# Performance work log

Measured on AMD Instinct MI355X. Metric: run time of the kernel, lower is better.

The kernel has to match this reference:

```python
import jax, jax.numpy as jnp
import numpy as np

TEMPERATURE = 0.1
EPS = 1e-12  # F.normalize eps


def setup_inputs() -> dict:
    key = jax.random.key(0)
    k1, k2 = jax.random.split(key)
    B, D = 4096, 128
    return {
        "x_i": jax.random.normal(k1, (B, D), dtype=jnp.float32),
        "x_j": jax.random.normal(k2, (B, D), dtype=jnp.float32),
    }


def _l2_normalize(x):
    n = jnp.sqrt(jnp.sum(x * x, axis=1, keepdims=True))
    return x / jnp.maximum(n, EPS)


def reference(x_i, x_j):
    B = x_i.shape[0]
    z = jnp.concatenate([_l2_normalize(x_i), _l2_normalize(x_j)], axis=0)  # [2B, D]
    # cosine similarity of unit-norm rows == dot product -> single GEMM
    sim = z @ z.T  # [2B, 2B]
    idx = jnp.arange(B)
    sim_ij = sim[idx, idx + B]   # diag(sim, +B)
    sim_ji = sim[idx + B, idx]   # diag(sim, -B)
    positives = jnp.concatenate([sim_ij, sim_ji], axis=0)  # [2B]
    neg_mask = 1.0 - jnp.eye(2 * B, dtype=sim.dtype)
    denominator = jnp.sum(neg_mask * jnp.exp(sim / TEMPERATURE), axis=1)  # [2B]
    # -log(exp(pos/t) / denom) = -(pos/t - log denom)
    loss_partial = jnp.log(denominator) - positives / TEMPERATURE
    return jnp.sum(loss_partial) / (2 * B)
```

## Files before the change

kernel.cpp:

```cpp
#include <hip/hip_runtime.h>
#include <stdint.h>

#define D_DIM 128
#define NROW 8192
#define L2EPS 1e-12f
#define SCALE_PRE 0.9495707f
#define LN2 0.6931471805599453f

typedef __attribute__((ext_vector_type(4))) int   i32x4;
typedef __attribute__((ext_vector_type(8))) int   i32x8;
typedef __attribute__((ext_vector_type(4))) float f32x4;

#define AS1 __attribute__((address_space(1)))
#define AS3 __attribute__((address_space(3)))

static __device__ inline void gload_lds16(const void* g, void* l) {
    __builtin_amdgcn_global_load_lds((const AS1 uint32_t*)g, (AS3 uint32_t*)l, 16, 0, 0);
}

static __device__ inline i32x8 cat8(i32x4 lo, i32x4 hi) {
    i32x8 r;
    r[0] = lo[0]; r[1] = lo[1]; r[2] = lo[2]; r[3] = lo[3];
    r[4] = hi[0]; r[5] = hi[1]; r[6] = hi[2]; r[7] = hi[3];
    return r;
}

static __device__ __forceinline__ float fexp2(float x) {
#if __has_builtin(__builtin_amdgcn_exp2f)
    return __builtin_amdgcn_exp2f(x);
#else
    float r;
    asm("v_exp_f32 %0, %1" : "=v"(r) : "v"(x));
    return r;
#endif
}

static __device__ __forceinline__ float dpp_row_sum16(float v) {
    union { float f; int i; } u, s;
    u.f = v;
    s.i = __builtin_amdgcn_update_dpp(0, u.i, 0x118, 0xF, 0xF, true); u.f += s.f;
    s.i = __builtin_amdgcn_update_dpp(0, u.i, 0x114, 0xF, 0xF, true); u.f += s.f;
    s.i = __builtin_amdgcn_update_dpp(0, u.i, 0x112, 0xF, 0xF, true); u.f += s.f;
    s.i = __builtin_amdgcn_update_dpp(0, u.i, 0x111, 0xF, 0xF, true); u.f += s.f;
    return u.f;
}

__global__ __launch_bounds__(256) void k_normalize(
        const float* __restrict__ xi, const float* __restrict__ xj,
        uint8_t* __restrict__ z8, float* __restrict__ rowacc,
        float* __restrict__ colacc, float* __restrict__ pos_acc,
        float* __restrict__ logsum, unsigned* __restrict__ done_ct) {
    const int wave = threadIdx.x >> 6;
    const int lane = threadIdx.x & 63;
    const int row = blockIdx.x * 4 + wave;
    const float* src = (row < 4096) ? (xi + (size_t)row * D_DIM)
                                    : (xj + (size_t)(row - 4096) * D_DIM);
    float2 v = *(const float2*)(src + lane * 2);
    float ss = v.x * v.x + v.y * v.y;
#pragma unroll
    for (int m = 32; m >= 1; m >>= 1) ss += __shfl_xor(ss, m, 64);
    const float scale = SCALE_PRE / fmaxf(sqrtf(ss), L2EPS);
    const int pk = __builtin_amdgcn_cvt_pk_fp8_f32(v.x * scale, v.y * scale, 0, false);
    *(ushort*)(z8 + (size_t)row * D_DIM + lane * 2) = (ushort)pk;

    if (blockIdx.x < 32)
        rowacc[blockIdx.x * 256 + threadIdx.x] = 0.0f;
    else if (blockIdx.x < 64)
        colacc[(blockIdx.x - 32) * 256 + threadIdx.x] = 0.0f;

    if (blockIdx.x == 0 && threadIdx.x == 0) {
        pos_acc[0] = 0.0f; logsum[0] = 0.0f; done_ct[0] = 0u;
    }
}

__global__ __launch_bounds__(256) void k_gemm(
        const uint8_t* __restrict__ z8, float* __restrict__ rowacc,
        float* __restrict__ colacc, float* __restrict__ pos_acc) {
    __shared__ __align__(16) uint8_t lds[32768];

    const int t = threadIdx.x;
    const int wave = t >> 6, lane = t & 63;
    const int quad = lane >> 4, lc = lane & 15;

    const int mb = blockIdx.x >> 6;
    const int rb = blockIdx.x & 63;
    const int rowbase = rb * 128;
    const bool diag = (mb == 16);
    const int c1 = diag ? rb : (rb + 2 * mb + 1) & 63;
    const int c2 = (rb + 2 * mb + 2) & 63;

    {
        const uint8_t* zb1 = z8 + (size_t)c1 * 128 * D_DIM;
#pragma unroll
        for (int q = 0; q < 4; q++) {
            const int s = q * 256 + t;
            const int r = s >> 3;
            const int g = (s & 7) ^ (r & 7);
            gload_lds16(zb1 + (size_t)r * D_DIM + g * 16, &lds[s * 16]);
        }
        if (!diag) {
            const uint8_t* zb2 = z8 + (size_t)c2 * 128 * D_DIM;
#pragma unroll
            for (int q = 0; q < 4; q++) {
                const int s = q * 256 + t;
                const int r = s >> 3;
                const int g = (s & 7) ^ (r & 7);
                gload_lds16(zb2 + (size_t)r * D_DIM + g * 16, &lds[16384 + s * 16]);
            }
        }
    }

    i32x8 afr[2];
    {
        const uint8_t* pa = z8 + (size_t)(rowbase + wave * 32 + lc) * D_DIM + quad * 32;
#pragma unroll
        for (int i = 0; i < 2; i++) {
            i32x4 lo = *(const i32x4*)(pa + i * 16 * D_DIM);
            i32x4 hi = *(const i32x4*)(pa + i * 16 * D_DIM + 16);
            afr[i] = cat8(lo, hi);
        }
    }

    asm volatile("s_waitcnt vmcnt(0)" ::: "memory");
    __syncthreads();

    float rs[2][4] = {{0.f,0.f,0.f,0.f},{0.f,0.f,0.f,0.f}};
    float cs[16];
#pragma unroll
    for (int j = 0; j < 16; j++) cs[j] = 0.f;
    float posp = 0.f;
    const int rl0 = wave * 32 + quad * 4;

#define MFMA_J(j, A0, A1)                                                     \
    i32x4 blo, bhi; {                                                         \
        const int rowb = ((j) * 16 + lc) * D_DIM;                             \
        blo = *(const i32x4*)&lds[rowb + (((quad * 2)     ^ (lc & 7)) * 16)]; \
        bhi = *(const i32x4*)&lds[rowb + (((quad * 2 + 1) ^ (lc & 7)) * 16)]; \
    }                                                                         \
    const i32x8 bfr = cat8(blo, bhi);                                         \
    f32x4 z4 = {0.f, 0.f, 0.f, 0.f};                                          \
    f32x4 A0 = __builtin_amdgcn_mfma_scale_f32_16x16x128_f8f6f4(              \
                   afr[0], bfr, z4, 0, 0, 0, 131, 0, 127);                    \
    f32x4 A1 = __builtin_amdgcn_mfma_scale_f32_16x16x128_f8f6f4(              \
                   afr[1], bfr, z4, 0, 0, 0, 131, 0, 127);

    if (!diag) {
#pragma unroll
        for (int j = 0; j < 8; j++) {
            MFMA_J(j, a0, a1)
#pragma unroll
            for (int r = 0; r < 4; r++) {
                const float e0 = fexp2(a0[r]);
                const float e1 = fexp2(a1[r]);
                rs[0][r] += e0;
                rs[1][r] += e1;
                cs[j] += e0 + e1;
            }
        }
        if (mb < 15) {
#pragma unroll
            for (int j = 8; j < 16; j++) {
                MFMA_J(j, a0, a1)
#pragma unroll
                for (int r = 0; r < 4; r++) {
                    const float e0 = fexp2(a0[r]);
                    const float e1 = fexp2(a1[r]);
                    rs[0][r] += e0;
                    rs[1][r] += e1;
                    cs[j] += e0 + e1;
                }
            }
        } else {
#pragma unroll
            for (int j = 8; j < 16; j++) {
                MFMA_J(j, a0, a1)
                const int clb = (j - 8) * 16 + lc;
#pragma unroll
                for (int i = 0; i < 2; i++)
#pragma unroll
                    for (int r = 0; r < 4; r++) {
                        const float s = (i ? a1 : a0)[r];
                        const float e = 0.5f * fexp2(s);
                        if (clb == rl0 + i * 16 + r) posp += s;
                        rs[i][r] += e;
                        cs[j] += e;
                    }
            }
        }
    } else {
#pragma unroll
        for (int j = 0; j < 8; j++) {
            MFMA_J(j, a0, a1)
            const int cl = j * 16 + lc;
#pragma unroll
            for (int i = 0; i < 2; i++)
#pragma unroll
                for (int r = 0; r < 4; r++) {
                    const float s = (i ? a1 : a0)[r];
                    const float e = (cl > rl0 + i * 16 + r) ? fexp2(s) : 0.f;
                    rs[i][r] += e;
                    cs[j] += e;
                }
        }
    }
#undef MFMA_J

#pragma unroll
    for (int i = 0; i < 2; i++)
#pragma unroll
        for (int r = 0; r < 4; r++) {
            const float v = dpp_row_sum16(rs[i][r]);
            if (lc == 15)
                atomicAdd(&rowacc[rowbase + rl0 + i * 16 + r], v);
        }

#pragma unroll
    for (int j = 0; j < 16; j++) {
        cs[j] += __shfl_xor(cs[j], 16, 64);
        cs[j] += __shfl_xor(cs[j], 32, 64);
    }
    if (quad == 0) {
#pragma unroll
        for (int j = 0; j < 16; j++) {
            if (diag && j >= 8) break;
            const int band = (j < 8) ? c1 : c2;
            atomicAdd(&colacc[band * 128 + (j & 7) * 16 + lc], cs[j]);
        }
    }

    if (mb == 15) {
#pragma unroll
        for (int mm = 32; mm >= 1; mm >>= 1) posp += __shfl_xor(posp, mm, 64);
        if (lane == 0) atomicAdd(pos_acc, posp);
    }
}

__global__ __launch_bounds__(256) void k_logsum(
        const float* __restrict__ rowacc, const float* __restrict__ colacc,
        float* __restrict__ pos_acc, float* __restrict__ logsum,
        unsigned* __restrict__ done_ct, float* __restrict__ out) {
    const int row = blockIdx.x * 256 + threadIdx.x;
    const float d = rowacc[row] + colacc[row];
    float v = __logf(d);
#pragma unroll
    for (int m = 32; m >= 1; m >>= 1) v += __shfl_xor(v, m, 64);
    if ((threadIdx.x & 63) == 0) atomicAdd(logsum, v);
    __threadfence();
    __syncthreads();
    if (threadIdx.x == 0) {
        const unsigned prev = atomicAdd(done_ct, 1u);
        if (prev == gridDim.x - 1) {
            __threadfence();
            const float ls = atomicAdd(logsum, 0.0f);
            const float pp = atomicAdd(pos_acc, 0.0f);
            out[0] = (ls - pp * LN2) / (float)NROW;
        }
    }
}

extern "C" void kernel_launch(void* const* d_in, const int* in_sizes, int n_in,
                              void* d_out, int out_size, void* d_ws, size_t ws_size,
                              hipStream_t stream) {
    const float* xi = (const float*)d_in[0];
    const float* xj = (const float*)d_in[1];
    uint8_t* z8 = (uint8_t*)d_ws;
    float* rowacc = (float*)(z8 + (size_t)NROW * D_DIM);
    float* colacc = rowacc + NROW;
    float* pos_acc = colacc + NROW;
    float* logsum = pos_acc + 1;
    unsigned* done_ct = (unsigned*)(logsum + 1);
    float* out = (float*)d_out;

    hipLaunchKernelGGL(k_normalize, dim3(NROW / 4), dim3(256), 0, stream,
                       xi, xj, z8, rowacc, colacc, pos_acc, logsum, done_ct);
    hipLaunchKernelGGL(k_gemm, dim3(17 * 64), dim3(256), 0, stream,
                       z8, rowacc, colacc, pos_acc);
    hipLaunchKernelGGL(k_logsum, dim3(NROW / 256), dim3(256), 0, stream,
                       rowacc, colacc, pos_acc, logsum, done_ct, out);
}
```

Measured before the change: 78.14 us.

## Use 512-thread GEMM blocks covering 256x256 tiles with split B-band loads

The symmetric-GEMM kernel moves from 256-thread blocks over 128x256 tiles to 512-thread blocks where eight waves cover two adjacent 128-row A bands against two B bands. The block schedule is remapped so that 512 off-diagonal blocks plus 64 diagonal blocks cover the triangle. The second B band's load is issued after the first and waited on separately, so compute on the first band can overlap the second load. The intent is to halve the block count and cut LDS traffic per output, at the cost of bigger blocks and a trickier mapping of the positive and half-weight tiles.

```diff
diff --git a/kernel.cpp b/kernel.cpp
--- a/kernel.cpp
+++ b/kernel.cpp
@@ -73,7 +73,7 @@
     }
 }
 
-__global__ __launch_bounds__(256) void k_gemm(
+__global__ __launch_bounds__(512) void k_gemm(
         const uint8_t* __restrict__ z8, float* __restrict__ rowacc,
         float* __restrict__ colacc, float* __restrict__ pos_acc) {
     __shared__ __align__(16) uint8_t lds[32768];
@@ -81,55 +81,57 @@
     const int t = threadIdx.x;
     const int wave = t >> 6, lane = t & 63;
     const int quad = lane >> 4, lc = lane & 15;
-
-    const int mb = blockIdx.x >> 6;
-    const int rb = blockIdx.x & 63;
-    const int rowbase = rb * 128;
-    const bool diag = (mb == 16);
-    const int c1 = diag ? rb : (rb + 2 * mb + 1) & 63;
-    const int c2 = (rb + 2 * mb + 2) & 63;
-
-    {
-        const uint8_t* zb1 = z8 + (size_t)c1 * 128 * D_DIM;
-#pragma unroll
-        for (int q = 0; q < 4; q++) {
-            const int s = q * 256 + t;
+    const int bid = blockIdx.x;
+
+    const f32x4 z4 = {0.f, 0.f, 0.f, 0.f};
+
+    if (bid < 512) {
+        const int mb = bid >> 6;
+        const int b  = bid & 63;
+        const int b1 = (b + 4 * mb + 2) & 63;
+        const int b2 = (b + 4 * mb + 4) & 63;
+
+#pragma unroll
+        for (int q = 0; q < 2; q++) {
+            const int s = q * 512 + t;
             const int r = s >> 3;
             const int g = (s & 7) ^ (r & 7);
-            gload_lds16(zb1 + (size_t)r * D_DIM + g * 16, &lds[s * 16]);
-        }
-        if (!diag) {
-            const uint8_t* zb2 = z8 + (size_t)c2 * 128 * D_DIM;
-#pragma unroll
-            for (int q = 0; q < 4; q++) {
-                const int s = q * 256 + t;
-                const int r = s >> 3;
-                const int g = (s & 7) ^ (r & 7);
-                gload_lds16(zb2 + (size_t)r * D_DIM + g * 16, &lds[16384 + s * 16]);
-            }
-        }
-    }
-
-    i32x8 afr[2];
-    {
-        const uint8_t* pa = z8 + (size_t)(rowbase + wave * 32 + lc) * D_DIM + quad * 32;
-#pragma unroll
-        for (int i = 0; i < 2; i++) {
-            i32x4 lo = *(const i32x4*)(pa + i * 16 * D_DIM);
-            i32x4 hi = *(const i32x4*)(pa + i * 16 * D_DIM + 16);
-            afr[i] = cat8(lo, hi);
-        }
-    }
-
-    asm volatile("s_waitcnt vmcnt(0)" ::: "memory");
-    __syncthreads();
-
-    float rs[2][4] = {{0.f,0.f,0.f,0.f},{0.f,0.f,0.f,0.f}};
-    float cs[16];
-#pragma unroll
-    for (int j = 0; j < 16; j++) cs[j] = 0.f;
-    float posp = 0.f;
-    const int rl0 = wave * 32 + quad * 4;
+            gload_lds16(z8 + (size_t)b1 * 128 * D_DIM + (size_t)r * D_DIM + g * 16,
+                        &lds[s * 16]);
+        }
+        asm volatile("" ::: "memory");
+
+        const int ab = (wave < 4) ? b : ((b + 1) & 63);
+        const int arow0 = ab * 128 + (wave & 3) * 32;
+        i32x8 afr[2];
+        {
+            const uint8_t* pa = z8 + (size_t)(arow0 + lc) * D_DIM + quad * 32;
+#pragma unroll
+            for (int i = 0; i < 2; i++) {
+                i32x4 lo = *(const i32x4*)(pa + i * 16 * D_DIM);
+                i32x4 hi = *(const i32x4*)(pa + i * 16 * D_DIM + 16);
+                afr[i] = cat8(lo, hi);
+            }
+        }
+        asm volatile("" ::: "memory");
+
+#pragma unroll
+        for (int q = 2; q < 4; q++) {
+            const int s = q * 512 + t;
+            const int r = s >> 3;
+            const int g = (s & 7) ^ (r & 7);
+            gload_lds16(z8 + (size_t)b2 * 128 * D_DIM + (size_t)(r - 128) * D_DIM + g * 16,
+                        &lds[s * 16]);
+        }
+
+        asm volatile("s_waitcnt vmcnt(2)" ::: "memory");
+        __syncthreads();
+
+        f32x4 rs4[2] = {z4, z4};
+        float cs[16];
+#pragma unroll
+        for (int j = 0; j < 16; j++) cs[j] = 0.f;
+        float posp = 0.f;
 
 #define MFMA_J(j, A0, A1)                                                     \
     i32x4 blo, bhi; {                                                         \
@@ -138,100 +140,162 @@
         bhi = *(const i32x4*)&lds[rowb + (((quad * 2 + 1) ^ (lc & 7)) * 16)]; \
     }                                                                         \
     const i32x8 bfr = cat8(blo, bhi);                                         \
-    f32x4 z4 = {0.f, 0.f, 0.f, 0.f};                                          \
     f32x4 A0 = __builtin_amdgcn_mfma_scale_f32_16x16x128_f8f6f4(              \
                    afr[0], bfr, z4, 0, 0, 0, 131, 0, 127);                    \
     f32x4 A1 = __builtin_amdgcn_mfma_scale_f32_16x16x128_f8f6f4(              \
                    afr[1], bfr, z4, 0, 0, 0, 131, 0, 127);
 
-    if (!diag) {
+#define CREDIT_FULL(j, A0, A1)                                                \
+    {                                                                         \
+        f32x4 ev0, ev1;                                                       \
+        ev0[0] = fexp2(A0[0]); ev0[1] = fexp2(A0[1]);                         \
+        ev0[2] = fexp2(A0[2]); ev0[3] = fexp2(A0[3]);                         \
+        ev1[0] = fexp2(A1[0]); ev1[1] = fexp2(A1[1]);                         \
+        ev1[2] = fexp2(A1[2]); ev1[3] = fexp2(A1[3]);                         \
+        rs4[0] += ev0;                                                        \
+        rs4[1] += ev1;                                                        \
+        cs[j] += ((ev0[0] + ev0[1]) + (ev0[2] + ev0[3]))                      \
+               + ((ev1[0] + ev1[1]) + (ev1[2] + ev1[3]));                     \
+    }
+
 #pragma unroll
         for (int j = 0; j < 8; j++) {
             MFMA_J(j, a0, a1)
-#pragma unroll
-            for (int r = 0; r < 4; r++) {
-                const float e0 = fexp2(a0[r]);
-                const float e1 = fexp2(a1[r]);
-                rs[0][r] += e0;
-                rs[1][r] += e1;
-                cs[j] += e0 + e1;
-            }
-        }
-        if (mb < 15) {
+            CREDIT_FULL(j, a0, a1)
+        }
+
+        asm volatile("s_waitcnt vmcnt(0)" ::: "memory");
+        __syncthreads();
+
+        if (mb < 7) {
 #pragma unroll
             for (int j = 8; j < 16; j++) {
                 MFMA_J(j, a0, a1)
-#pragma unroll
-                for (int r = 0; r < 4; r++) {
-                    const float e0 = fexp2(a0[r]);
-                    const float e1 = fexp2(a1[r]);
-                    rs[0][r] += e0;
-                    rs[1][r] += e1;
-                    cs[j] += e0 + e1;
+                CREDIT_FULL(j, a0, a1)
+            }
+        } else {
+            if (wave < 4) {
+#pragma unroll
+                for (int j = 8; j < 16; j++) {
+                    MFMA_J(j, a0, a1)
+                    const int clb = (j - 8) * 16 + lc;
+                    const int rl0 = wave * 32 + quad * 4;
+#pragma unroll
+                    for (int i = 0; i < 2; i++)
+#pragma unroll
+                        for (int r = 0; r < 4; r++) {
+                            const float s = (i ? a1 : a0)[r];
+                            const float e = 0.5f * fexp2(s);
+                            if (clb == rl0 + i * 16 + r) posp += s;
+                            rs4[i][r] += e;
+                            cs[j] += e;
+                        }
                 }
-            }
-        } else {
-#pragma unroll
-            for (int j = 8; j < 16; j++) {
-                MFMA_J(j, a0, a1)
-                const int clb = (j - 8) * 16 + lc;
-#pragma unroll
-                for (int i = 0; i < 2; i++)
-#pragma unroll
-                    for (int r = 0; r < 4; r++) {
-                        const float s = (i ? a1 : a0)[r];
-                        const float e = 0.5f * fexp2(s);
-                        if (clb == rl0 + i * 16 + r) posp += s;
-                        rs[i][r] += e;
-                        cs[j] += e;
-                    }
-            }
-        }
-    } else {
-#pragma unroll
-        for (int j = 0; j < 8; j++) {
-            MFMA_J(j, a0, a1)
-            const int cl = j * 16 + lc;
-#pragma unroll
-            for (int i = 0; i < 2; i++)
-#pragma unroll
-                for (int r = 0; r < 4; r++) {
-                    const float s = (i ? a1 : a0)[r];
-                    const float e = (cl > rl0 + i * 16 + r) ? fexp2(s) : 0.f;
-                    rs[i][r] += e;
-                    cs[j] += e;
+            } else {
+#pragma unroll
+                for (int j = 8; j < 16; j++) {
+                    MFMA_J(j, a0, a1)
+                    CREDIT_FULL(j, a0, a1)
                 }
-        }
-    }
+            }
+        }
+#undef CREDIT_FULL
 #undef MFMA_J
 
 #pragma unroll
-    for (int i = 0; i < 2; i++)
+        for (int i = 0; i < 2; i++)
+#pragma unroll
+            for (int r = 0; r < 4; r++) {
+                const float v = dpp_row_sum16(rs4[i][r]);
+                if (lc == 15)
+                    atomicAdd(&rowacc[arow0 + i * 16 + quad * 4 + r], v);
+            }
+
+#pragma unroll
+        for (int j = 0; j < 16; j++) {
+            cs[j] += __shfl_xor(cs[j], 16, 64);
+            cs[j] += __shfl_xor(cs[j], 32, 64);
+        }
+        if (quad == 0) {
+#pragma unroll
+            for (int j = 0; j < 16; j++) {
+                const int band = (j < 8) ? b1 : b2;
+                atomicAdd(&colacc[band * 128 + (j & 7) * 16 + lc], cs[j]);
+            }
+        }
+
+        if (mb == 7 && wave < 4) {
+#pragma unroll
+            for (int mm = 32; mm >= 1; mm >>= 1) posp += __shfl_xor(posp, mm, 64);
+            if (lane == 0) atomicAdd(pos_acc, posp);
+        }
+        return;
+    }
+
+    const int rb = bid - 512;
+    {
+        const uint8_t* zb = z8 + (size_t)rb * 128 * D_DIM;
+#pragma unroll
+        for (int q = 0; q < 2; q++) {
+            const int s = q * 512 + t;
+            const int r = s >> 3;
+            const int g = (s & 7) ^ (r & 7);
+            gload_lds16(zb + (size_t)r * D_DIM + g * 16, &lds[s * 16]);
+        }
+    }
+
+    i32x8 afr;
+    {
+        const uint8_t* pa = z8 + (size_t)(rb * 128 + wave * 16 + lc) * D_DIM + quad * 32;
+        i32x4 lo = *(const i32x4*)pa;
+        i32x4 hi = *(const i32x4*)(pa + 16);
+        afr = cat8(lo, hi);
+    }
+
+    asm volatile("s_waitcnt vmcnt(0)" ::: "memory");
+    __syncthreads();
+
+    f32x4 rs4 = z4;
+    float cs[8];
+#pragma unroll
+    for (int j = 0; j < 8; j++) cs[j] = 0.f;
+    const int rl0 = wave * 16 + quad * 4;
+
+#pragma unroll
+    for (int j = 0; j < 8; j++) {
+        i32x4 blo, bhi; {
+            const int rowb = (j * 16 + lc) * D_DIM;
+            blo = *(const i32x4*)&lds[rowb + (((quad * 2)     ^ (lc & 7)) * 16)];
+            bhi = *(const i32x4*)&lds[rowb + (((quad * 2 + 1) ^ (lc & 7)) * 16)];
+        }
+        const i32x8 bfr = cat8(blo, bhi);
+        f32x4 a0 = __builtin_amdgcn_mfma_scale_f32_16x16x128_f8f6f4(
+                       afr, bfr, z4, 0, 0, 0, 131, 0, 127);
+        const int cl = j * 16 + lc;
 #pragma unroll
         for (int r = 0; r < 4; r++) {
-            const float v = dpp_row_sum16(rs[i][r]);
-            if (lc == 15)
-                atomicAdd(&rowacc[rowbase + rl0 + i * 16 + r], v);
-        }
-
-#pragma unroll
-    for (int j = 0; j < 16; j++) {
+            const float e = (cl > rl0 + r) ? fexp2(a0[r]) : 0.f;
+            rs4[r] += e;
+            cs[j] += e;
+        }
+    }
+
+#pragma unroll
+    for (int r = 0; r < 4; r++) {
+        const float v = dpp_row_sum16(rs4[r]);
+        if (lc == 15)
+            atomicAdd(&rowacc[rb * 128 + rl0 + r], v);
+    }
+
+#pragma unroll
+    for (int j = 0; j < 8; j++) {
         cs[j] += __shfl_xor(cs[j], 16, 64);
         cs[j] += __shfl_xor(cs[j], 32, 64);
     }
     if (quad == 0) {
 #pragma unroll
-        for (int j = 0; j < 16; j++) {
-            if (diag && j >= 8) break;
-            const int band = (j < 8) ? c1 : c2;
-            atomicAdd(&colacc[band * 128 + (j & 7) * 16 + lc], cs[j]);
-        }
-    }
-
-    if (mb == 15) {
-#pragma unroll
-        for (int mm = 32; mm >= 1; mm >>= 1) posp += __shfl_xor(posp, mm, 64);
-        if (lane == 0) atomicAdd(pos_acc, posp);
+        for (int j = 0; j < 8; j++)
+            atomicAdd(&colacc[rb * 128 + j * 16 + lc], cs[j]);
     }
 }
 
@@ -273,7 +337,7 @@
 
     hipLaunchKernelGGL(k_normalize, dim3(NROW / 4), dim3(256), 0, stream,
                        xi, xj, z8, rowacc, colacc, pos_acc, logsum, done_ct);
-    hipLaunchKernelGGL(k_gemm, dim3(17 * 64), dim3(256), 0, stream,
+    hipLaunchKernelGGL(k_gemm, dim3(512 + 64), dim3(512), 0, stream,
                        z8, rowacc, colacc, pos_acc);
     hipLaunchKernelGGL(k_logsum, dim3(NROW / 256), dim3(256), 0, stream,
                        rowacc, colacc, pos_acc, logsum, done_ct, out);
```

Result: faster. 76.00 us, median of 2 (-2.7%).
